# Kernel tuning notes

Measured on AMD Instinct MI355X. Metric: run time of the kernel, lower is better.

## Reference

```python
import jax, jax.numpy as jnp
import numpy as np

N_COARSE = 64
N_FINE = 64
EPS = 1e-5

BS, N_RAYS = 1, 131072


def setup_inputs() -> dict:
    key = jax.random.key(0)
    k0, k1, k2, k3, k4, k5 = jax.random.split(key, 6)
    origins = jax.random.normal(k0, (BS, N_RAYS, 3), dtype=jnp.float32)
    dirs = jax.random.normal(k1, (BS, N_RAYS, 3), dtype=jnp.float32)
    dirs = dirs / jnp.linalg.norm(dirs, axis=-1, keepdims=True)
    near = 2.0 + 0.5 * jax.random.uniform(k2, (BS, N_RAYS, 1), dtype=jnp.float32)
    far = 6.0 + 0.5 * jax.random.uniform(k3, (BS, N_RAYS, 1), dtype=jnp.float32)
    rays = jnp.concatenate([origins, dirs, near, far], axis=-1)  # (bs, n_rays, 8)
    sigmas_coarse = jax.random.normal(k4, (BS, N_RAYS, N_COARSE), dtype=jnp.float32)
    rgbs_coarse = jax.random.uniform(k5, (BS, N_RAYS, N_COARSE, 3), dtype=jnp.float32)
    k6, k7 = jax.random.split(jax.random.fold_in(key, 1), 2)
    sigmas_fine = jax.random.normal(k6, (BS, N_RAYS, N_COARSE + N_FINE), dtype=jnp.float32)
    rgbs_fine = jax.random.uniform(k7, (BS, N_RAYS, N_COARSE + N_FINE, 3), dtype=jnp.float32)
    return {
        "rays": rays,
        "sigmas_coarse": sigmas_coarse,
        "rgbs_coarse": rgbs_coarse,
        "sigmas_fine": sigmas_fine,
        "rgbs_fine": rgbs_fine,
    }


def composite(rays, z_samp, sigmas, rgbs):
    """Alpha compositing along the sample axis (white background, far=inf)."""
    deltas = z_samp[..., 1:] - z_samp[..., :-1]
    delta_inf = jnp.full_like(deltas[..., :1], 1e10)
    deltas = jnp.concatenate([deltas, delta_inf], axis=-1)  # (bs, n_rays, K)
    alphas = 1.0 - jnp.exp(-deltas * jax.nn.relu(sigmas))
    shifted = jnp.concatenate(
        [jnp.ones_like(alphas[..., :1]), 1.0 - alphas + 1e-10], axis=-1)
    T = jnp.cumprod(shifted, axis=-1)  # transmittance
    weights = alphas * T[..., :-1]
    weights_sum = jnp.sum(weights, axis=-1, keepdims=True)
    rgb_final = jnp.sum(weights[..., None] * rgbs, axis=-2)
    depth_final = jnp.sum(weights * z_samp, axis=-1, keepdims=True)
    far = rays[..., 7:8]
    depth_final = depth_final + (1.0 - weights_sum) * far  # white_bkgd
    rgb_final = rgb_final + 1.0 - weights_sum
    return weights, rgb_final, depth_final, weights_sum


def sample_fine(bins, weights):
    """Deterministic inverse-CDF importance sampling (det=True, perturb=0)."""
    bs, n_rays = bins.shape[:2]
    w = jax.lax.stop_gradient(weights) + EPS  # (bs, n_rays, Kc-2)
    pdf = w / jnp.sum(w, axis=-1, keepdims=True)
    cdf = jnp.cumsum(pdf, axis=-1)
    cdf = jnp.concatenate([jnp.zeros_like(cdf[..., :1]), cdf], axis=-1)  # (.., Kc-1)
    u = jnp.broadcast_to(jnp.linspace(0.0, 1.0, N_FINE, dtype=cdf.dtype),
                         (bs, n_rays, N_FINE))
    n_bins = cdf.shape[-1]
    inds = jax.vmap(lambda c, uu: jnp.searchsorted(c, uu, side='right'))(
        cdf.reshape(-1, n_bins), u.reshape(-1, N_FINE)).reshape(bs, n_rays, N_FINE)
    below = jnp.maximum(inds - 1, 0)
    above = jnp.minimum(inds, N_COARSE - 2)
    cdf_b = jnp.take_along_axis(cdf, below, axis=-1)
    cdf_a = jnp.take_along_axis(cdf, above, axis=-1)
    bin_b = jnp.take_along_axis(bins, below, axis=-1)
    bin_a = jnp.take_along_axis(bins, above, axis=-1)
    denom = cdf_a - cdf_b
    denom = jnp.where(denom < EPS, 1.0, denom)
    z_fine = bin_b + (u - cdf_b) / denom * (bin_a - bin_b)
    return jax.lax.stop_gradient(z_fine)


def reference(rays, sigmas_coarse, rgbs_coarse, sigmas_fine, rgbs_fine):
    near, far = rays[..., 6:7], rays[..., 7:8]
    # sample_coarse, lindisp=True branch: linear blend of near/far, perturb=0
    step = 1.0 / N_COARSE
    t = jnp.linspace(0.0, 1.0 - step, N_COARSE, dtype=rays.dtype)
    z_coarse = near * (1.0 - t) + far * t  # (bs, n_rays, Kc)

    weights, rgbs, depths, alphas = composite(rays, z_coarse, sigmas_coarse, rgbs_coarse)

    bins = 0.5 * (z_coarse[..., :-1] + z_coarse[..., 1:])  # (.., Kc-1)
    z_fine = sample_fine(bins, weights[..., 1:-1])  # (.., Kf)
    z_combine = jnp.sort(jnp.concatenate([z_coarse, z_fine], axis=-1), axis=-1)

    weights_f, rgbs_f, depths_f, alphas_f = composite(rays, z_combine, sigmas_fine, rgbs_fine)
    # output dict: rgbs, alphas, depths (+ fine variants)
    return rgbs, alphas, depths, rgbs_f, alphas_f, depths_f
```

## Files before the change

### kernel.cpp

```cpp
#include <hip/hip_runtime.h>

#define EPS_F 1e-5f

__device__ __forceinline__ float wave_sum64(float v) {
  #pragma unroll
  for (int off = 32; off; off >>= 1) v += __shfl_xor(v, off);
  return v;
}

__global__ __launch_bounds__(256) void nerf_volrend(
    const float* __restrict__ rays,
    const float* __restrict__ sigc,
    const float* __restrict__ rgbc,
    const float* __restrict__ sigf,
    const float* __restrict__ rgbf,
    float* __restrict__ out, int n_rays)
{
  const int wave = threadIdx.x >> 6;
  const int lane = threadIdx.x & 63;
  const int ray  = (blockIdx.x << 2) + wave;

  __shared__ float s_cdf [4][64];
  __shared__ float s_bins[4][64];
  __shared__ float s_zc  [4][64];
  __shared__ float s_zf  [4][64];
  __shared__ float s_zcb [4][128];

  const float nearv = rays[ray*8 + 6];
  const float farv  = rays[ray*8 + 7];

  const float t = (float)lane * 0.015625f;
  const float z = nearv * (1.0f - t) + farv * t;
  const float znext = __shfl_down(z, 1);
  const float delta = (lane == 63) ? 1e10f : (znext - z);
  float sgv = sigc[ray*64 + lane];
  sgv = fmaxf(sgv, 0.0f);
  const float a = 1.0f - __expf(-delta * sgv);
  const float sh = 1.0f - a + 1e-10f;

  float pin = sh;
  #pragma unroll
  for (int off = 1; off < 64; off <<= 1) {
    float tmp = __shfl_up(pin, off);
    if (lane >= off) pin *= tmp;
  }
  float T = __shfl_up(pin, 1);
  if (lane == 0) T = 1.0f;
  const float w = a * T;

  const float r0 = rgbc[ray*192 + lane*3 + 0];
  const float r1 = rgbc[ray*192 + lane*3 + 1];
  const float r2 = rgbc[ray*192 + lane*3 + 2];

  const float wsum = wave_sum64(w);
  const float cR = wave_sum64(w * r0);
  const float cG = wave_sum64(w * r1);
  const float cB = wave_sum64(w * r2);
  const float cD = wave_sum64(w * z);

  if (lane == 0) {
    out[ray*3 + 0]      = cR + 1.0f - wsum;
    out[ray*3 + 1]      = cG + 1.0f - wsum;
    out[ray*3 + 2]      = cB + 1.0f - wsum;
    out[n_rays*3 + ray] = wsum;
    out[n_rays*4 + ray] = cD + (1.0f - wsum) * farv;
  }

  const float wnext = __shfl_down(w, 1);
  const float wp = (lane < 62) ? (wnext + EPS_F) : 0.0f;
  const float wpsum = wave_sum64(wp);
  const float pdf = wp / wpsum;
  float csum = pdf;
  #pragma unroll
  for (int off = 1; off < 64; off <<= 1) {
    float tmp = __shfl_up(csum, off);
    if (lane >= off) csum += tmp;
  }

  s_zc[wave][lane] = z;
  if (lane < 63) s_bins[wave][lane] = 0.5f * (z + znext);
  if (lane < 62) s_cdf[wave][lane + 1] = csum;
  if (lane == 0) s_cdf[wave][0] = 0.0f;
  __syncthreads();

  const float* cdf  = s_cdf[wave];
  const float* bins = s_bins[wave];
  const float u = (lane == 63) ? 1.0f : (float)lane * (1.0f / 63.0f);
  int pos = 0;
  #pragma unroll
  for (int stp = 32; stp; stp >>= 1) {
    int np = pos + stp;
    if (np <= 63 && cdf[np - 1] <= u) pos = np;
  }
  const int below = max(pos - 1, 0);
  const int above = min(pos, 62);
  const float cdf_b = cdf[below], cdf_a = cdf[above];
  const float bin_b = bins[below], bin_a = bins[above];
  float dn = cdf_a - cdf_b;
  if (dn < EPS_F) dn = 1.0f;
  const float zf = bin_b + (u - cdf_b) / dn * (bin_a - bin_b);
  s_zf[wave][lane] = zf;
  __syncthreads();

  const float* zcl = s_zc[wave];
  const float* zfl = s_zf[wave];
  int cf = 0;
  #pragma unroll
  for (int stp = 64; stp; stp >>= 1) {
    int np = cf + stp;
    if (np <= 64 && zfl[np - 1] < z) cf = np;
  }
  int cc = 0;
  #pragma unroll
  for (int stp = 64; stp; stp >>= 1) {
    int np = cc + stp;
    if (np <= 64 && zcl[np - 1] <= zf) cc = np;
  }
  s_zcb[wave][lane + cf] = z;
  s_zcb[wave][lane + cc] = zf;
  __syncthreads();

  const float* zcb = s_zcb[wave];
  const float z0 = zcb[2*lane];
  const float z1 = zcb[2*lane + 1];
  const int   i2 = (lane == 63) ? 0 : (2*lane + 2);
  const float z2 = zcb[i2];
  const float d0 = z1 - z0;
  const float d1 = (lane == 63) ? 1e10f : (z2 - z1);

  const float2 sgf = ((const float2*)(sigf + (size_t)ray*128))[lane];
  const float s0 = fmaxf(sgf.x, 0.0f);
  const float s1 = fmaxf(sgf.y, 0.0f);
  const float a0 = 1.0f - __expf(-d0 * s0);
  const float a1 = 1.0f - __expf(-d1 * s1);
  const float t0 = 1.0f - a0 + 1e-10f;
  const float t1 = 1.0f - a1 + 1e-10f;

  float pp = t0 * t1;
  #pragma unroll
  for (int off = 1; off < 64; off <<= 1) {
    float tmp = __shfl_up(pp, off);
    if (lane >= off) pp *= tmp;
  }
  float Pex = __shfl_up(pp, 1);
  if (lane == 0) Pex = 1.0f;
  const float w0 = a0 * Pex;
  const float w1 = a1 * Pex * t0;

  const float* rb = rgbf + (size_t)ray*384 + lane*6;
  const float2 rA = *(const float2*)(rb + 0);
  const float2 rB = *(const float2*)(rb + 2);
  const float2 rC = *(const float2*)(rb + 4);

  const float fR = wave_sum64(w0 * rA.x + w1 * rB.y);
  const float fG = wave_sum64(w0 * rA.y + w1 * rC.x);
  const float fB = wave_sum64(w0 * rB.x + w1 * rC.y);
  const float fD = wave_sum64(w0 * z0   + w1 * z1);
  const float fW = wave_sum64(w0 + w1);

  if (lane == 0) {
    out[n_rays*5 + ray*3 + 0] = fR + 1.0f - fW;
    out[n_rays*5 + ray*3 + 1] = fG + 1.0f - fW;
    out[n_rays*5 + ray*3 + 2] = fB + 1.0f - fW;
    out[n_rays*8 + ray]       = fW;
    out[n_rays*9 + ray]       = fD + (1.0f - fW) * farv;
  }
}

extern "C" void kernel_launch(void* const* d_in, const int* in_sizes, int n_in,
                              void* d_out, int out_size, void* d_ws, size_t ws_size,
                              hipStream_t stream) {
  const float* rays = (const float*)d_in[0];
  const float* sigc = (const float*)d_in[1];
  const float* rgbc = (const float*)d_in[2];
  const float* sigf = (const float*)d_in[3];
  const float* rgbf = (const float*)d_in[4];
  float* out = (float*)d_out;
  const int n_rays = in_sizes[0] / 8;
  const int blocks = n_rays / 4;
  nerf_volrend<<<blocks, 256, 0, stream>>>(rays, sigc, rgbc, sigf, rgbf, out, n_rays);
}
```

Baseline: 418.5 us.

## Use DPP wave scans and drop block barriers with analytic merge indices

Replaces the shuffle-based scans and reductions with DPP row_shr/row_bcast scan sequences and a readlane for totals. It removes all __syncthreads by relying on wave-local LDS use, and computes bin values and the coarse merge position analytically from near/far instead of storing them in shared memory and binary searching. The fine-sample merge position now searches the per-lane cc array by lane index. Risks are floating-point mismatches between the analytic floor index and the original comparison-based sort near bin boundaries, and dependence on implicit wave-level LDS ordering without a barrier.

```diff
diff --git a/kernel.cpp b/kernel.cpp
--- a/kernel.cpp
+++ b/kernel.cpp
@@ -2,10 +2,30 @@
 
 #define EPS_F 1e-5f
 
-__device__ __forceinline__ float wave_sum64(float v) {
-  #pragma unroll
-  for (int off = 32; off; off >>= 1) v += __shfl_xor(v, off);
-  return v;
+#define DPPF(old, x, ctrl, rm, bm) \
+  __int_as_float(__builtin_amdgcn_update_dpp(__float_as_int(old), __float_as_int(x), ctrl, rm, bm, false))
+
+__device__ __forceinline__ float scan_add64(float x) {
+  x += DPPF(0.0f, x, 0x111, 0xf, 0xf);
+  x += DPPF(0.0f, x, 0x112, 0xf, 0xf);
+  x += DPPF(0.0f, x, 0x114, 0xf, 0xf);
+  x += DPPF(0.0f, x, 0x118, 0xf, 0xf);
+  x += DPPF(0.0f, x, 0x142, 0xa, 0xf);
+  x += DPPF(0.0f, x, 0x143, 0xc, 0xf);
+  return x;
+}
+__device__ __forceinline__ float scan_mul64(float x) {
+  x *= DPPF(1.0f, x, 0x111, 0xf, 0xf);
+  x *= DPPF(1.0f, x, 0x112, 0xf, 0xf);
+  x *= DPPF(1.0f, x, 0x114, 0xf, 0xf);
+  x *= DPPF(1.0f, x, 0x118, 0xf, 0xf);
+  x *= DPPF(1.0f, x, 0x142, 0xa, 0xf);
+  x *= DPPF(1.0f, x, 0x143, 0xc, 0xf);
+  return x;
+}
+__device__ __forceinline__ float wave_total(float x) {
+  float s = scan_add64(x);
+  return __int_as_float(__builtin_amdgcn_readlane(__float_as_int(s), 63));
 }
 
 __global__ __launch_bounds__(256) void nerf_volrend(
@@ -20,30 +40,24 @@
   const int lane = threadIdx.x & 63;
   const int ray  = (blockIdx.x << 2) + wave;
 
-  __shared__ float s_cdf [4][64];
-  __shared__ float s_bins[4][64];
-  __shared__ float s_zc  [4][64];
-  __shared__ float s_zf  [4][64];
-  __shared__ float s_zcb [4][128];
+  __shared__ float s_cdf[4][64];
+  __shared__ int   s_cc [4][64];
+  __shared__ float s_zcb[4][128];
 
   const float nearv = rays[ray*8 + 6];
   const float farv  = rays[ray*8 + 7];
 
-  const float t = (float)lane * 0.015625f;
-  const float z = nearv * (1.0f - t) + farv * t;
-  const float znext = __shfl_down(z, 1);
+  const float t  = (float)lane * 0.015625f;
+  const float tn = (float)(lane + 1) * 0.015625f;
+  const float z     = nearv * (1.0f - t)  + farv * t;
+  const float znext = nearv * (1.0f - tn) + farv * tn;
   const float delta = (lane == 63) ? 1e10f : (znext - z);
   float sgv = sigc[ray*64 + lane];
   sgv = fmaxf(sgv, 0.0f);
-  const float a = 1.0f - __expf(-delta * sgv);
+  const float a  = 1.0f - __expf(-delta * sgv);
   const float sh = 1.0f - a + 1e-10f;
 
-  float pin = sh;
-  #pragma unroll
-  for (int off = 1; off < 64; off <<= 1) {
-    float tmp = __shfl_up(pin, off);
-    if (lane >= off) pin *= tmp;
-  }
+  const float pin = scan_mul64(sh);
   float T = __shfl_up(pin, 1);
   if (lane == 0) T = 1.0f;
   const float w = a * T;
@@ -52,11 +66,11 @@
   const float r1 = rgbc[ray*192 + lane*3 + 1];
   const float r2 = rgbc[ray*192 + lane*3 + 2];
 
-  const float wsum = wave_sum64(w);
-  const float cR = wave_sum64(w * r0);
-  const float cG = wave_sum64(w * r1);
-  const float cB = wave_sum64(w * r2);
-  const float cD = wave_sum64(w * z);
+  const float wsum = wave_total(w);
+  const float cR = wave_total(w * r0);
+  const float cG = wave_total(w * r1);
+  const float cB = wave_total(w * r2);
+  const float cD = wave_total(w * z);
 
   if (lane == 0) {
     out[ray*3 + 0]      = cR + 1.0f - wsum;
@@ -67,24 +81,14 @@
   }
 
   const float wnext = __shfl_down(w, 1);
-  const float wp = (lane < 62) ? (wnext + EPS_F) : 0.0f;
-  const float wpsum = wave_sum64(wp);
-  const float pdf = wp / wpsum;
-  float csum = pdf;
-  #pragma unroll
-  for (int off = 1; off < 64; off <<= 1) {
-    float tmp = __shfl_up(csum, off);
-    if (lane >= off) csum += tmp;
-  }
+  const float wp    = (lane < 62) ? (wnext + EPS_F) : 0.0f;
+  const float wpsum = wave_total(wp);
+  const float csum  = scan_add64(wp / wpsum);
 
-  s_zc[wave][lane] = z;
-  if (lane < 63) s_bins[wave][lane] = 0.5f * (z + znext);
   if (lane < 62) s_cdf[wave][lane + 1] = csum;
   if (lane == 0) s_cdf[wave][0] = 0.0f;
-  __syncthreads();
 
-  const float* cdf  = s_cdf[wave];
-  const float* bins = s_bins[wave];
+  const float* cdf = s_cdf[wave];
   const float u = (lane == 63) ? 1.0f : (float)lane * (1.0f / 63.0f);
   int pos = 0;
   #pragma unroll
@@ -95,36 +99,33 @@
   const int below = max(pos - 1, 0);
   const int above = min(pos, 62);
   const float cdf_b = cdf[below], cdf_a = cdf[above];
-  const float bin_b = bins[below], bin_a = bins[above];
+  const float tb  = (float)below * 0.015625f, tb1 = (float)(below + 1) * 0.015625f;
+  const float ta  = (float)above * 0.015625f, ta1 = (float)(above + 1) * 0.015625f;
+  const float bin_b = 0.5f * ((nearv*(1.0f-tb)  + farv*tb)  + (nearv*(1.0f-tb1) + farv*tb1));
+  const float bin_a = 0.5f * ((nearv*(1.0f-ta)  + farv*ta)  + (nearv*(1.0f-ta1) + farv*ta1));
   float dn = cdf_a - cdf_b;
   if (dn < EPS_F) dn = 1.0f;
   const float zf = bin_b + (u - cdf_b) / dn * (bin_a - bin_b);
-  s_zf[wave][lane] = zf;
-  __syncthreads();
 
-  const float* zcl = s_zc[wave];
-  const float* zfl = s_zf[wave];
+  const float inv_step = 64.0f / (farv - nearv);
+  int cc = (int)floorf((zf - nearv) * inv_step) + 1;
+  cc = min(max(cc, 0), 64);
+  s_cc[wave][lane] = cc;
+  s_zcb[wave][lane + cc] = zf;
+
+  const int* ccl = s_cc[wave];
   int cf = 0;
   #pragma unroll
   for (int stp = 64; stp; stp >>= 1) {
     int np = cf + stp;
-    if (np <= 64 && zfl[np - 1] < z) cf = np;
-  }
-  int cc = 0;
-  #pragma unroll
-  for (int stp = 64; stp; stp >>= 1) {
-    int np = cc + stp;
-    if (np <= 64 && zcl[np - 1] <= zf) cc = np;
+    if (np <= 64 && ccl[np - 1] <= lane) cf = np;
   }
   s_zcb[wave][lane + cf] = z;
-  s_zcb[wave][lane + cc] = zf;
-  __syncthreads();
 
   const float* zcb = s_zcb[wave];
-  const float z0 = zcb[2*lane];
-  const float z1 = zcb[2*lane + 1];
-  const int   i2 = (lane == 63) ? 0 : (2*lane + 2);
-  const float z2 = zcb[i2];
+  const float2 zp = ((const float2*)zcb)[lane];
+  const float z0 = zp.x, z1 = zp.y;
+  const float z2 = zcb[(lane == 63) ? 127 : (2*lane + 2)];
   const float d0 = z1 - z0;
   const float d1 = (lane == 63) ? 1e10f : (z2 - z1);
 
@@ -136,12 +137,7 @@
   const float t0 = 1.0f - a0 + 1e-10f;
   const float t1 = 1.0f - a1 + 1e-10f;
 
-  float pp = t0 * t1;
-  #pragma unroll
-  for (int off = 1; off < 64; off <<= 1) {
-    float tmp = __shfl_up(pp, off);
-    if (lane >= off) pp *= tmp;
-  }
+  const float pp = scan_mul64(t0 * t1);
   float Pex = __shfl_up(pp, 1);
   if (lane == 0) Pex = 1.0f;
   const float w0 = a0 * Pex;
@@ -152,11 +148,11 @@
   const float2 rB = *(const float2*)(rb + 2);
   const float2 rC = *(const float2*)(rb + 4);
 
-  const float fR = wave_sum64(w0 * rA.x + w1 * rB.y);
-  const float fG = wave_sum64(w0 * rA.y + w1 * rC.x);
-  const float fB = wave_sum64(w0 * rB.x + w1 * rC.y);
-  const float fD = wave_sum64(w0 * z0   + w1 * z1);
-  const float fW = wave_sum64(w0 + w1);
+  const float fR = wave_total(w0 * rA.x + w1 * rB.y);
+  const float fG = wave_total(w0 * rA.y + w1 * rC.x);
+  const float fB = wave_total(w0 * rB.x + w1 * rC.y);
+  const float fD = wave_total(w0 * z0   + w1 * z1);
+  const float fW = wave_total(w0 + w1);
 
   if (lane == 0) {
     out[n_rays*5 + ray*3 + 0] = fR + 1.0f - fW;
```

Result: faster. 399.5 us (-4.5%).
